# Kernel tuning notes

Measured on AMD Instinct MI355X. Metric: run time of the kernel, lower is better.

## Reference

```python
import jax, jax.numpy as jnp
import numpy as np

N = 50000      # nodes
E = 800000     # edges (before self loops)
F_IN = 512     # input feature dim (num_features)
D = 128        # hidden_dim
NBLK = 3       # num_layers - 1
EPS = 1e-5


def _layernorm(x, g, b):
    mu = x.mean(-1, keepdims=True)
    var = ((x - mu) ** 2).mean(-1, keepdims=True)
    return (x - mu) / jnp.sqrt(var + EPS) * g + b


def _gatv2(x, Wl, bl, Wr, br, att, bias, src, dst, n):
    # PyG GATv2Conv, heads=1, eval mode (attention dropout off), self loops in src/dst
    xl = x @ Wl + bl                      # [N, D] messages (x_j side)
    xr = x @ Wr + br                      # [N, D] target side (x_i)
    e = jax.nn.leaky_relu(xl[src] + xr[dst], negative_slope=0.2)  # [E', D]
    score = e @ att                       # [E']
    smax = jax.ops.segment_max(score, dst, num_segments=n)
    ex = jnp.exp(score - smax[dst])
    denom = jax.ops.segment_sum(ex, dst, num_segments=n)
    alpha = ex / denom[dst]               # segment softmax over incoming edges
    out = jax.ops.segment_sum(alpha[:, None] * xl[src], dst, num_segments=n)
    return out + bias


def setup_inputs() -> dict:
    key = jax.random.key(0)
    ks = jax.random.split(key, 32)
    w = lambda k, shape: (jax.random.normal(k, shape, jnp.float32) * 0.02)
    p = {}
    p["x"] = jax.random.normal(ks[0], (N, F_IN), jnp.float32)
    p["edge_index"] = jax.random.randint(ks[1], (2, E), 0, N)
    p["emb_W"] = w(ks[2], (F_IN, D)); p["emb_b"] = jnp.zeros((D,), jnp.float32)
    p["ln1_g"] = jnp.ones((NBLK, D), jnp.float32); p["ln1_b"] = jnp.zeros((NBLK, D), jnp.float32)
    p["gat_Wl"] = w(ks[3], (NBLK, D, D)); p["gat_bl"] = jnp.zeros((NBLK, D), jnp.float32)
    p["gat_Wr"] = w(ks[4], (NBLK, D, D)); p["gat_br"] = jnp.zeros((NBLK, D), jnp.float32)
    p["gat_att"] = w(ks[5], (NBLK, D)); p["gat_bias"] = jnp.zeros((NBLK, D), jnp.float32)
    for i in range(NBLK):
        h = D * (i + 1)  # mlp_ratio = level = i+1
        p[f"mlp_w1_{i}"] = w(ks[6 + 2 * i], (D, h))
        p[f"mlp_w2_{i}"] = w(ks[7 + 2 * i], (h, D))
    p["attn_Wa"] = w(ks[12], (D, D)); p["attn_ba"] = jnp.zeros((D,), jnp.float32)
    p["attn_Wb"] = w(ks[13], (D, D)); p["attn_bb"] = jnp.zeros((D,), jnp.float32)
    p["attn_Wc"] = w(ks[14], (D, 1)); p["attn_bc"] = jnp.zeros((1,), jnp.float32)
    p["rho_W"] = w(ks[15], (D, D)); p["rho_b"] = jnp.zeros((D,), jnp.float32)
    p["cls_W"] = w(ks[16], (D, 4)); p["cls_b"] = jnp.zeros((4,), jnp.float32)
    return p


def reference(x, edge_index, emb_W, emb_b, ln1_g, ln1_b, gat_Wl, gat_bl, gat_Wr, gat_br,
              gat_att, gat_bias, mlp_w1_0, mlp_w2_0, mlp_w1_1, mlp_w2_1, mlp_w1_2, mlp_w2_2,
              attn_Wa, attn_ba, attn_Wb, attn_bb, attn_Wc, attn_bc, rho_W, rho_b, cls_W, cls_b):
    n = x.shape[0]
    sl = jnp.arange(n, dtype=edge_index.dtype)
    src = jnp.concatenate([edge_index[0], sl])  # add self loops (GATv2Conv default)
    dst = jnp.concatenate([edge_index[1], sl])
    h = jax.nn.relu(x @ emb_W + emb_b)          # embedding (dropout off)
    mlps = [(mlp_w1_0, mlp_w2_0), (mlp_w1_1, mlp_w2_1), (mlp_w1_2, mlp_w2_2)]
    for i in range(NBLK):
        hn = _layernorm(h, ln1_g[i], ln1_b[i])
        h = h + _gatv2(hn, gat_Wl[i], gat_bl[i], gat_Wr[i], gat_br[i], gat_att[i], gat_bias[i], src, dst, n)
        w1, w2 = mlps[i]
        # NOTE: original forward applies channel_mix directly on x (norm2 is unused)
        h = h + jax.nn.gelu(h @ w1, approximate=False) @ w2
    # Attn_Net_Gated pooling
    a = jnp.tanh(h @ attn_Wa + attn_ba)
    b = jax.nn.sigmoid(h @ attn_Wb + attn_bb)
    A = ((a * b) @ attn_Wc + attn_bc).T          # [1, N]
    h_path = jax.nn.softmax(A, axis=1) @ h       # [1, D]
    hr = jax.nn.relu(h_path @ rho_W + rho_b)
    logits = hr @ cls_W + cls_b                  # [1, 4]
    Y_hat = jnp.argmax(logits, axis=1, keepdims=True)
    hazards = jax.nn.sigmoid(logits)
    S = jnp.cumprod(1.0 - hazards, axis=1)
    return (hazards, S, Y_hat, logits)
```

## Files before the change

kernel.cpp:

```cpp
#include <hip/hip_runtime.h>
#include <math.h>


#define D 128
#define NBLK 3
#define STG_STRIDE 132
#define S16 136
#define ROWS 128
#define BT 512

typedef __attribute__((ext_vector_type(8))) short bf16x8;
typedef __attribute__((ext_vector_type(4))) float f32x4;

static __device__ __forceinline__ float bf2f(unsigned short u) {
    union { unsigned i; float f; } c; c.i = ((unsigned)u) << 16; return c.f;
}
static __device__ __forceinline__ unsigned short f2bf(float f) {
    union { float f; unsigned i; } c; c.f = f;
    unsigned r = c.i + 0x7fff + ((c.i >> 16) & 1);
    return (unsigned short)(r >> 16);
}
static __device__ __forceinline__ void gl16(const unsigned short* g, unsigned short* l) {
    __builtin_amdgcn_global_load_lds((const __attribute__((address_space(1))) void*)g,
                                     (__attribute__((address_space(3))) void*)l, 16, 0, 0);
}
static __device__ __forceinline__ float gelu_f(float x) {
    return 0.5f * x * (1.f + erff(x * 0.70710678118654752f));
}

__global__ void zero_k(int* deg, int* fill, float* red, int n) {
    int i = blockIdx.x * blockDim.x + threadIdx.x;
    if (i < n) { deg[i] = 0; fill[i] = 0; }
    if (i < 132) red[i] = 0.f;
}

__global__ void hist_k(const int* __restrict__ dst, int* __restrict__ deg, int E) {
    int e = blockIdx.x * blockDim.x + threadIdx.x;
    if (e < E) atomicAdd(&deg[dst[e]], 1);
}

__global__ __launch_bounds__(256) void blockscan_k(const int* __restrict__ deg,
                                                   int* __restrict__ rowptr,
                                                   int* __restrict__ bsum, int n) {
    __shared__ int tmp[256];
    const int tid = threadIdx.x;
    const int i = blockIdx.x * 256 + tid;
    int v = (i < n) ? deg[i] : 0;
    tmp[tid] = v;
    __syncthreads();
#pragma unroll
    for (int off = 1; off < 256; off <<= 1) {
        int t = (tid >= off) ? tmp[tid - off] : 0;
        __syncthreads();
        tmp[tid] += t;
        __syncthreads();
    }
    if (i < n) rowptr[i + 1] = tmp[tid];
    if (tid == 255) bsum[blockIdx.x] = tmp[255];
}

__global__ __launch_bounds__(256) void scansums_k(int* __restrict__ bsum, int nb) {
    __shared__ int tmp[256];
    const int tid = threadIdx.x;
    int v = (tid < nb) ? bsum[tid] : 0;
    tmp[tid] = v;
    __syncthreads();
#pragma unroll
    for (int off = 1; off < 256; off <<= 1) {
        int t = (tid >= off) ? tmp[tid - off] : 0;
        __syncthreads();
        tmp[tid] += t;
        __syncthreads();
    }
    if (tid < nb) bsum[tid] = tmp[tid];
}

__global__ __launch_bounds__(256) void addoff_k(int* __restrict__ rowptr,
                                                const int* __restrict__ bsum, int n) {
    int i = blockIdx.x * 256 + threadIdx.x;
    if (i == 0) rowptr[0] = 0;
    if (i < n && blockIdx.x > 0) rowptr[i + 1] += bsum[blockIdx.x - 1];
}

__global__ void scatter_k(const int* __restrict__ src, const int* __restrict__ dst,
                          const int* __restrict__ rowptr, int* __restrict__ fill,
                          int* __restrict__ esrc, int E) {
    int e = blockIdx.x * blockDim.x + threadIdx.x;
    if (e < E) {
        int d = dst[e];
        int pos = rowptr[d] + atomicAdd(&fill[d], 1);
        esrc[pos] = src[e];
    }
}

struct WDesc { const float* s; unsigned short* d; int K; int M; };
struct WPack { WDesc w[21]; };

__global__ __launch_bounds__(256) void wprep_k(WPack p) {
    WDesc d = p.w[blockIdx.y];
    const int nc = d.K / 32;
    const int chunks = (d.M / 16) * nc * 64;
    for (int i = blockIdx.x * 256 + threadIdx.x; i < chunks; i += gridDim.x * 256) {
        const int l = i & 63;
        const int c = (i >> 6) % nc;
        const int t = i / (64 * nc);
        const int m = t * 16 + (l & 15);
        const int kb = c * 32 + ((l >> 4) & 3) * 8;
#pragma unroll
        for (int j = 0; j < 8; ++j)
            d.d[(size_t)i * 8 + j] = f2bf(d.s[(size_t)(kb + j) * d.M + m]);
    }
}

__global__ __launch_bounds__(256) void bcat_k(const float* bl, const float* br,
                                              const float* ba, const float* bb,
                                              float* sb) {
    const int t = threadIdx.x;
    for (int i = 0; i < 3; ++i)
        sb[i * 256 + t] = (t < 128) ? bl[i * 128 + t] : br[i * 128 + t - 128];
    sb[3 * 256 + t] = (t < 128) ? ba[t] : bb[t - 128];
}


static __device__ __forceinline__ void stage_blob(const unsigned short* src,
                                                  unsigned short* wls, int tid) {
#pragma unroll
    for (int i = 0; i < 4; ++i) {
        const int idx = i * BT + tid;
        gl16(src + (size_t)idx * 8, &wls[idx * 8]);
    }
}

static __device__ __forceinline__ void ln_row(float av[4][8], const float* lng,
                                              const float* lnb, int q) {
    float s = 0.f;
#pragma unroll
    for (int c = 0; c < 4; ++c)
#pragma unroll
        for (int j = 0; j < 8; ++j) s += av[c][j];
    s += __shfl_xor(s, 16, 64); s += __shfl_xor(s, 32, 64);
    const float mu = s * (1.f / 128.f);
    float vv = 0.f;
#pragma unroll
    for (int c = 0; c < 4; ++c)
#pragma unroll
        for (int j = 0; j < 8; ++j) { const float dd = av[c][j] - mu; vv += dd * dd; }
    vv += __shfl_xor(vv, 16, 64); vv += __shfl_xor(vv, 32, 64);
    const float rs = rsqrtf(vv * (1.f / 128.f) + 1e-5f);
#pragma unroll
    for (int c = 0; c < 4; ++c) {
        const int kb = c * 32 + q * 8;
        const float4 g0 = *(const float4*)(lng + kb);
        const float4 g1 = *(const float4*)(lng + kb + 4);
        const float4 b0 = *(const float4*)(lnb + kb);
        const float4 b1 = *(const float4*)(lnb + kb + 4);
        const float gg[8] = {g0.x, g0.y, g0.z, g0.w, g1.x, g1.y, g1.z, g1.w};
        const float bb[8] = {b0.x, b0.y, b0.z, b0.w, b1.x, b1.y, b1.z, b1.w};
#pragma unroll
        for (int j = 0; j < 8; ++j)
            av[c][j] = (av[c][j] - mu) * rs * gg[j] + bb[j];
    }
}

static __device__ __forceinline__ void gatproj(const bf16x8 xfr[4],
                                               const unsigned short* gatc,
                                               const float* sb256,
                                               unsigned short* X,
                                               unsigned short* wls,
                                               int rowbase, int w, int l, int N,
                                               int tid) {
    const int q = l >> 4, l15 = l & 15;
#pragma unroll
    for (int rnd = 0; rnd < 2; ++rnd) {
        __syncthreads();
        stage_blob(gatc + (size_t)rnd * 16384, wls, tid);
        f32x4 acc[8];
#pragma unroll
        for (int t = 0; t < 8; ++t) acc[t] = (f32x4){0.f, 0.f, 0.f, 0.f};
        __syncthreads();
#pragma unroll
        for (int c = 0; c < 4; ++c)
#pragma unroll
            for (int t = 0; t < 8; ++t) {
                const bf16x8 bfr = *(const bf16x8*)&wls[((t * 4 + c) * 64 + l) * 8];
                acc[t] = __builtin_amdgcn_mfma_f32_16x16x32_bf16(xfr[c], bfr, acc[t], 0, 0, 0);
            }
#pragma unroll
        for (int t = 0; t < 8; ++t) {
            const int col = rnd * 128 + t * 16 + l15;
            const float bv = sb256[col];
#pragma unroll
            for (int rr = 0; rr < 4; ++rr) {
                const int row = rowbase + w * 16 + q * 4 + rr;
                if (row < N) X[(size_t)row * 256 + col] = f2bf(acc[t][rr] + bv);
            }
        }
    }
}

__global__ __launch_bounds__(BT) void start_k(const float* __restrict__ x,
                                              const unsigned short* __restrict__ embc,
                                              const float* __restrict__ emb_b,
                                              const unsigned short* __restrict__ gatc,
                                              const float* __restrict__ lng,
                                              const float* __restrict__ lnb,
                                              const float* __restrict__ sb256,
                                              float* __restrict__ H,
                                              unsigned short* __restrict__ X, int N) {
    __shared__ __align__(16) char smem[ROWS * STG_STRIDE * 4];
    unsigned short* wls = (unsigned short*)smem;
    float* stg = (float*)smem;
    const int tid = threadIdx.x;
    const int w = tid >> 6, l = tid & 63, q = l >> 4, l15 = l & 15;
    const int rowbase = blockIdx.x * ROWS;
    int r = rowbase + w * 16 + l15;
    const bool rv = r < N; if (!rv) r = N - 1;

    f32x4 accH[8];
#pragma unroll
    for (int t = 0; t < 8; ++t) accH[t] = (f32x4){0.f, 0.f, 0.f, 0.f};

#pragma unroll
    for (int rnd = 0; rnd < 4; ++rnd) {
        if (rnd) __syncthreads();
        stage_blob(embc + (size_t)rnd * 16384, wls, tid);
        bf16x8 afr[4];
#pragma unroll
        for (int c = 0; c < 4; ++c) {
            const float* ap = x + (size_t)r * 512 + rnd * 128 + c * 32 + q * 8;
            const float4 v0 = *(const float4*)ap;
            const float4 v1 = *(const float4*)(ap + 4);
            afr[c][0] = (short)f2bf(v0.x); afr[c][1] = (short)f2bf(v0.y);
            afr[c][2] = (short)f2bf(v0.z); afr[c][3] = (short)f2bf(v0.w);
            afr[c][4] = (short)f2bf(v1.x); afr[c][5] = (short)f2bf(v1.y);
            afr[c][6] = (short)f2bf(v1.z); afr[c][7] = (short)f2bf(v1.w);
        }
        __syncthreads();
#pragma unroll
        for (int c = 0; c < 4; ++c)
#pragma unroll
            for (int t = 0; t < 8; ++t) {
                const bf16x8 bfr = *(const bf16x8*)&wls[((t * 4 + c) * 64 + l) * 8];
                accH[t] = __builtin_amdgcn_mfma_f32_16x16x32_bf16(afr[c], bfr, accH[t], 0, 0, 0);
            }
    }

    __syncthreads();
#pragma unroll
    for (int t = 0; t < 8; ++t) {
        const int col = t * 16 + l15;
        const float bv = emb_b[col];
#pragma unroll
        for (int rr = 0; rr < 4; ++rr) {
            const int row = rowbase + w * 16 + q * 4 + rr;
            const float hv = fmaxf(accH[t][rr] + bv, 0.f);
            if (row < N) H[(size_t)row * D + col] = hv;
            stg[(w * 16 + q * 4 + rr) * STG_STRIDE + col] = hv;
        }
    }
    __syncthreads();

    float av[4][8];
#pragma unroll
    for (int c = 0; c < 4; ++c)
#pragma unroll
        for (int j = 0; j < 8; ++j)
            av[c][j] = stg[(w * 16 + l15) * STG_STRIDE + c * 32 + q * 8 + j];
    ln_row(av, lng, lnb, q);
    bf16x8 xfr[4];
#pragma unroll
    for (int c = 0; c < 4; ++c)
#pragma unroll
        for (int j = 0; j < 8; ++j) xfr[c][j] = (short)f2bf(av[c][j]);

    gatproj(xfr, gatc, sb256, X, wls, rowbase, w, l, N, tid);
}

template <int NMR>
__global__ __launch_bounds__(BT) void bridge_k(float* __restrict__ H,
                                               const unsigned short* __restrict__ w1c,
                                               const unsigned short* __restrict__ w2c,
                                               const unsigned short* __restrict__ gatc,
                                               const float* __restrict__ lng,
                                               const float* __restrict__ lnb,
                                               const float* __restrict__ sb256,
                                               unsigned short* __restrict__ X, int N) {
    __shared__ __align__(16) char smem[ROWS * STG_STRIDE * 4];
    unsigned short* wls   = (unsigned short*)smem;
    unsigned short* stg16 = (unsigned short*)(smem + 32768);
    float*          stgF  = (float*)smem;
    const int tid = threadIdx.x;
    const int w = tid >> 6, l = tid & 63, q = l >> 4, l15 = l & 15;
    const int rowbase = blockIdx.x * ROWS;
    int r = rowbase + w * 16 + l15;
    const bool rv = r < N; if (!rv) r = N - 1;

    float av[4][8];
    bf16x8 afr[4];
#pragma unroll
    for (int c = 0; c < 4; ++c) {
        const float* ap = H + (size_t)r * D + c * 32 + q * 8;
        const float4 v0 = *(const float4*)ap;
        const float4 v1 = *(const float4*)(ap + 4);
        av[c][0] = v0.x; av[c][1] = v0.y; av[c][2] = v0.z; av[c][3] = v0.w;
        av[c][4] = v1.x; av[c][5] = v1.y; av[c][6] = v1.z; av[c][7] = v1.w;
#pragma unroll
        for (int j = 0; j < 8; ++j) afr[c][j] = (short)f2bf(av[c][j]);
    }

    f32x4 accH[8];
#pragma unroll
    for (int t = 0; t < 8; ++t) accH[t] = (f32x4){0.f, 0.f, 0.f, 0.f};

#pragma unroll
    for (int rnd = 0; rnd < NMR; ++rnd) {
        __syncthreads();
        stage_blob(w1c + (size_t)rnd * 16384, wls, tid);
        f32x4 accT[8];
#pragma unroll
        for (int t = 0; t < 8; ++t) accT[t] = (f32x4){0.f, 0.f, 0.f, 0.f};
        __syncthreads();
#pragma unroll
        for (int c = 0; c < 4; ++c)
#pragma unroll
            for (int t = 0; t < 8; ++t) {
                const bf16x8 bfr = *(const bf16x8*)&wls[((t * 4 + c) * 64 + l) * 8];
                accT[t] = __builtin_amdgcn_mfma_f32_16x16x32_bf16(afr[c], bfr, accT[t], 0, 0, 0);
            }
        __syncthreads();
#pragma unroll
        for (int t = 0; t < 8; ++t)
#pragma unroll
            for (int rr = 0; rr < 4; ++rr)
                stg16[(w * 16 + q * 4 + rr) * S16 + t * 16 + l15] = f2bf(gelu_f(accT[t][rr]));
        stage_blob(w2c + (size_t)rnd * 16384, wls, tid);
        __syncthreads();
        bf16x8 tfr[4];
#pragma unroll
        for (int c = 0; c < 4; ++c)
            tfr[c] = *(const bf16x8*)&stg16[(w * 16 + l15) * S16 + c * 32 + q * 8];
#pragma unroll
        for (int c = 0; c < 4; ++c)
#pragma unroll
            for (int t = 0; t < 8; ++t) {
                const bf16x8 bfr = *(const bf16x8*)&wls[((t * 4 + c) * 64 + l) * 8];
                accH[t] = __builtin_amdgcn_mfma_f32_16x16x32_bf16(tfr[c], bfr, accH[t], 0, 0, 0);
            }
    }

    __syncthreads();
#pragma unroll
    for (int t = 0; t < 8; ++t)
#pragma unroll
        for (int rr = 0; rr < 4; ++rr)
            stgF[(w * 16 + q * 4 + rr) * STG_STRIDE + t * 16 + l15] = accH[t][rr];
    __syncthreads();
#pragma unroll
    for (int c = 0; c < 4; ++c)
#pragma unroll
        for (int j = 0; j < 8; ++j)
            av[c][j] += stgF[(w * 16 + l15) * STG_STRIDE + c * 32 + q * 8 + j];

    if (rv) {
#pragma unroll
        for (int c = 0; c < 4; ++c) {
            float* hp = H + (size_t)r * D + c * 32 + q * 8;
            *(float4*)hp       = make_float4(av[c][0], av[c][1], av[c][2], av[c][3]);
            *(float4*)(hp + 4) = make_float4(av[c][4], av[c][5], av[c][6], av[c][7]);
        }
    }

    ln_row(av, lng, lnb, q);
    bf16x8 xfr[4];
#pragma unroll
    for (int c = 0; c < 4; ++c)
#pragma unroll
        for (int j = 0; j < 8; ++j) xfr[c][j] = (short)f2bf(av[c][j]);

    gatproj(xfr, gatc, sb256, X, wls, rowbase, w, l, N, tid);
}

__global__ __launch_bounds__(BT) void head_k(const float* __restrict__ H,
                                             const unsigned short* __restrict__ w1c,
                                             const unsigned short* __restrict__ w2c,
                                             const unsigned short* __restrict__ attc,
                                             const float* __restrict__ sb256,
                                             const float* __restrict__ Wc,
                                             const float* __restrict__ bc,
                                             float* __restrict__ red, int N) {
    __shared__ __align__(16) char smem[ROWS * STG_STRIDE * 4];
    unsigned short* wls   = (unsigned short*)smem;
    unsigned short* stg16 = (unsigned short*)(smem + 32768);
    float*          stgF  = (float*)smem;
    __shared__ float sacc[8][128];
    __shared__ float sdn[8];
    const int tid = threadIdx.x;
    const int w = tid >> 6, l = tid & 63, q = l >> 4, l15 = l & 15;
    const int rowbase = blockIdx.x * ROWS;
    int r = rowbase + w * 16 + l15;
    if (r > N - 1) r = N - 1;

    float av[4][8];
    bf16x8 afr[4];
#pragma unroll
    for (int c = 0; c < 4; ++c) {
        const float* ap = H + (size_t)r * D + c * 32 + q * 8;
        const float4 v0 = *(const float4*)ap;
        const float4 v1 = *(const float4*)(ap + 4);
        av[c][0] = v0.x; av[c][1] = v0.y; av[c][2] = v0.z; av[c][3] = v0.w;
        av[c][4] = v1.x; av[c][5] = v1.y; av[c][6] = v1.z; av[c][7] = v1.w;
#pragma unroll
        for (int j = 0; j < 8; ++j) afr[c][j] = (short)f2bf(av[c][j]);
    }

    f32x4 accH[8];
#pragma unroll
    for (int t = 0; t < 8; ++t) accH[t] = (f32x4){0.f, 0.f, 0.f, 0.f};

#pragma unroll
    for (int rnd = 0; rnd < 3; ++rnd) {
        __syncthreads();
        stage_blob(w1c + (size_t)rnd * 16384, wls, tid);
        f32x4 accT[8];
#pragma unroll
        for (int t = 0; t < 8; ++t) accT[t] = (f32x4){0.f, 0.f, 0.f, 0.f};
        __syncthreads();
#pragma unroll
        for (int c = 0; c < 4; ++c)
#pragma unroll
            for (int t = 0; t < 8; ++t) {
                const bf16x8 bfr = *(const bf16x8*)&wls[((t * 4 + c) * 64 + l) * 8];
                accT[t] = __builtin_amdgcn_mfma_f32_16x16x32_bf16(afr[c], bfr, accT[t], 0, 0, 0);
            }
        __syncthreads();
#pragma unroll
        for (int t = 0; t < 8; ++t)
#pragma unroll
            for (int rr = 0; rr < 4; ++rr)
                stg16[(w * 16 + q * 4 + rr) * S16 + t * 16 + l15] = f2bf(gelu_f(accT[t][rr]));
        stage_blob(w2c + (size_t)rnd * 16384, wls, tid);
        __syncthreads();
        bf16x8 tfr[4];
#pragma unroll
        for (int c = 0; c < 4; ++c)
            tfr[c] = *(const bf16x8*)&stg16[(w * 16 + l15) * S16 + c * 32 + q * 8];
#pragma unroll
        for (int c = 0; c < 4; ++c)
#pragma unroll
            for (int t = 0; t < 8; ++t) {
                const bf16x8 bfr = *(const bf16x8*)&wls[((t * 4 + c) * 64 + l) * 8];
                accH[t] = __builtin_amdgcn_mfma_f32_16x16x32_bf16(tfr[c], bfr, accH[t], 0, 0, 0);
            }
    }

    __syncthreads();
#pragma unroll
    for (int t = 0; t < 8; ++t)
#pragma unroll
        for (int rr = 0; rr < 4; ++rr)
            stgF[(w * 16 + q * 4 + rr) * STG_STRIDE + t * 16 + l15] = accH[t][rr];
    __syncthreads();
#pragma unroll
    for (int c = 0; c < 4; ++c)
#pragma unroll
        for (int j = 0; j < 8; ++j)
            av[c][j] += stgF[(w * 16 + l15) * STG_STRIDE + c * 32 + q * 8 + j];
#pragma unroll
    for (int c = 0; c < 4; ++c)
#pragma unroll
        for (int j = 0; j < 8; ++j) afr[c][j] = (short)f2bf(av[c][j]);

    float th[8][4];
    f32x4 acc[8];
#pragma unroll
    for (int rnd = 0; rnd < 2; ++rnd) {
        __syncthreads();
        stage_blob(attc + (size_t)rnd * 16384, wls, tid);
#pragma unroll
        for (int t = 0; t < 8; ++t) acc[t] = (f32x4){0.f, 0.f, 0.f, 0.f};
        __syncthreads();
#pragma unroll
        for (int c = 0; c < 4; ++c)
#pragma unroll
            for (int t = 0; t < 8; ++t) {
                const bf16x8 bfr = *(const bf16x8*)&wls[((t * 4 + c) * 64 + l) * 8];
                acc[t] = __builtin_amdgcn_mfma_f32_16x16x32_bf16(afr[c], bfr, acc[t], 0, 0, 0);
            }
        if (rnd == 0) {
#pragma unroll
            for (int t = 0; t < 8; ++t) {
                const float bv = sb256[t * 16 + l15];
#pragma unroll
                for (int rr = 0; rr < 4; ++rr) th[t][rr] = tanhf(acc[t][rr] + bv);
            }
        }
    }

    float pa[4] = {0.f, 0.f, 0.f, 0.f};
#pragma unroll
    for (int t = 0; t < 8; ++t) {
        const float bv = sb256[128 + t * 16 + l15];
        const float wcv = Wc[t * 16 + l15];
#pragma unroll
        for (int rr = 0; rr < 4; ++rr) {
            const float sg = 1.f / (1.f + __expf(-(acc[t][rr] + bv)));
            pa[rr] = fmaf(th[t][rr] * sg, wcv, pa[rr]);
        }
    }
#pragma unroll
    for (int m = 1; m < 16; m <<= 1)
#pragma unroll
        for (int rr = 0; rr < 4; ++rr) pa[rr] += __shfl_xor(pa[rr], m, 64);

    const float bcv = bc[0];
    float wgt[4];
#pragma unroll
    for (int rr = 0; rr < 4; ++rr) {
        const int row = rowbase + w * 16 + q * 4 + rr;
        wgt[rr] = (row < N) ? __expf(pa[rr] + bcv) : 0.f;
    }
    float s = wgt[0] + wgt[1] + wgt[2] + wgt[3];
    s += __shfl_xor(s, 16, 64);
    s += __shfl_xor(s, 32, 64);
    if (l == 0) sdn[w] = s;

    const int sl = ((l15 >> 2) << 4);
    float wv[4];
#pragma unroll
    for (int rr = 0; rr < 4; ++rr) wv[rr] = __shfl(wgt[rr], sl, 64);
    const int rsel = l15 & 3;
    const float wm = (rsel == 0) ? wv[0] : (rsel == 1) ? wv[1] : (rsel == 2) ? wv[2] : wv[3];

#pragma unroll
    for (int c = 0; c < 4; ++c) {
        float pv[8];
#pragma unroll
        for (int j = 0; j < 8; ++j) pv[j] = wm * av[c][j];
#pragma unroll
        for (int m = 1; m < 16; m <<= 1)
#pragma unroll
            for (int j = 0; j < 8; ++j) pv[j] += __shfl_xor(pv[j], m, 64);
        if (l15 == 0) {
#pragma unroll
            for (int j = 0; j < 8; ++j) sacc[w][c * 32 + q * 8 + j] = pv[j];
        }
    }
    __syncthreads();
    if (tid < 128) {
        float tot = 0.f;
#pragma unroll
        for (int ww = 0; ww < 8; ++ww) tot += sacc[ww][tid];
        atomicAdd(&red[tid], tot);
    }
    if (tid == 0) {
        float ds = 0.f;
#pragma unroll
        for (int ww = 0; ww < 8; ++ww) ds += sdn[ww];
        atomicAdd(&red[128], ds);
    }
}

__global__ __launch_bounds__(256) void gat3_k(const unsigned short* __restrict__ X,
                                              const float* __restrict__ att,
                                              const float* __restrict__ gbias,
                                              const int* __restrict__ rowptr,
                                              const int* __restrict__ esrc,
                                              float* __restrict__ H, int n) {
    const int l = threadIdx.x & 63;
    const int node = blockIdx.x * 4 + (threadIdx.x >> 6);
    if (node >= n) return;
    const int q = l >> 4;
    const int d0 = (l & 15) * 8;

    float a8[8], xr[8], xs[8];
    {
        const float4 t0 = *(const float4*)&att[d0];
        const float4 t1 = *(const float4*)&att[d0 + 4];
        a8[0] = t0.x; a8[1] = t0.y; a8[2] = t0.z; a8[3] = t0.w;
        a8[4] = t1.x; a8[5] = t1.y; a8[6] = t1.z; a8[7] = t1.w;
        const bf16x8 uxs = *(const bf16x8*)&X[(size_t)node * 256 + d0];
        const bf16x8 uxr = *(const bf16x8*)&X[(size_t)node * 256 + 128 + d0];
#pragma unroll
        for (int j = 0; j < 8; ++j) {
            xs[j] = bf2f((unsigned short)uxs[j]);
            xr[j] = bf2f((unsigned short)uxr[j]);
        }
    }

    float sc = 0.f;
#pragma unroll
    for (int j = 0; j < 8; ++j) {
        const float e = xs[j] + xr[j];
        sc = fmaf(a8[j], fmaxf(e, 0.2f * e), sc);
    }
#pragma unroll
    for (int m = 1; m < 16; m <<= 1) sc += __shfl_xor(sc, m, 64);
    const float wself = __expf(sc);
    float dsum = (q == 0) ? wself : 0.f;
    float acc[8];
#pragma unroll
    for (int j = 0; j < 8; ++j) acc[j] = (q == 0) ? wself * xs[j] : 0.f;

    const int p1 = rowptr[node + 1];
    int p = rowptr[node] + q;
    bool v0 = p < p1, v1 = p + 4 < p1, v2 = p + 8 < p1;
    int i2 = v2 ? esrc[p + 8] : 0;
    bf16x8 u0, u1;
    if (v0) u0 = *(const bf16x8*)&X[(size_t)esrc[p] * 256 + d0];
    if (v1) u1 = *(const bf16x8*)&X[(size_t)esrc[p + 4] * 256 + d0];
    while (v0) {
        bf16x8 u2;
        if (v2) u2 = *(const bf16x8*)&X[(size_t)i2 * 256 + d0];
        const bool v3 = p + 12 < p1;
        const int i3 = v3 ? esrc[p + 12] : 0;

        float xl[8];
#pragma unroll
        for (int j = 0; j < 8; ++j) xl[j] = bf2f((unsigned short)u0[j]);
        float e_sc = 0.f;
#pragma unroll
        for (int j = 0; j < 8; ++j) {
            const float e = xl[j] + xr[j];
            e_sc = fmaf(a8[j], fmaxf(e, 0.2f * e), e_sc);
        }
#pragma unroll
        for (int m = 1; m < 16; m <<= 1) e_sc += __shfl_xor(e_sc, m, 64);
        const float wgt = __expf(e_sc);
        dsum += wgt;
#pragma unroll
        for (int j = 0; j < 8; ++j) acc[j] = fmaf(wgt, xl[j], acc[j]);

        u0 = u1; u1 = u2; i2 = i3;
        v0 = v1; v1 = v2; v2 = v3;
        p += 4;
    }

#pragma unroll
    for (int m = 16; m < 64; m <<= 1) {
        dsum += __shfl_xor(dsum, m, 64);
#pragma unroll
        for (int j = 0; j < 8; ++j) acc[j] += __shfl_xor(acc[j], m, 64);
    }

    if (q == 0) {
        const float inv = 1.f / dsum;
        const size_t o = (size_t)node * D + d0;
        float4 h0 = *(const float4*)&H[o];
        float4 h1 = *(const float4*)&H[o + 4];
        float hv[8] = {h0.x, h0.y, h0.z, h0.w, h1.x, h1.y, h1.z, h1.w};
#pragma unroll
        for (int j = 0; j < 8; ++j) hv[j] += acc[j] * inv + gbias[d0 + j];
        *(float4*)&H[o]     = make_float4(hv[0], hv[1], hv[2], hv[3]);
        *(float4*)&H[o + 4] = make_float4(hv[4], hv[5], hv[6], hv[7]);
    }
}

__global__ __launch_bounds__(128) void final_k(const float* __restrict__ red,
                                               const float* __restrict__ rho_W,
                                               const float* __restrict__ rho_b,
                                               const float* __restrict__ cls_W,
                                               const float* __restrict__ cls_b,
                                               float* __restrict__ out) {
    __shared__ float hp[128];
    __shared__ float hr[128];
    __shared__ float lg[4];
    const int t = threadIdx.x;
    hp[t] = red[t] / red[128];
    __syncthreads();
    float s = rho_b[t];
    for (int k = 0; k < 128; ++k) s = fmaf(hp[k], rho_W[k * 128 + t], s);
    hr[t] = fmaxf(s, 0.f);
    __syncthreads();
    if (t < 4) {
        float l = cls_b[t];
        for (int k = 0; k < 128; ++k) l = fmaf(hr[k], cls_W[k * 4 + t], l);
        lg[t] = l;
    }
    __syncthreads();
    if (t == 0) {
        float hz[4], S[4];
        for (int c = 0; c < 4; ++c) hz[c] = 1.f / (1.f + expf(-lg[c]));
        S[0] = 1.f - hz[0];
        for (int c = 1; c < 4; ++c) S[c] = S[c - 1] * (1.f - hz[c]);
        int am = 0; float bm = lg[0];
        for (int c = 1; c < 4; ++c) if (lg[c] > bm) { bm = lg[c]; am = c; }
        out[0] = hz[0]; out[1] = hz[1]; out[2] = hz[2]; out[3] = hz[3];
        out[4] = S[0];  out[5] = S[1];  out[6] = S[2];  out[7] = S[3];
        out[8] = (float)am;
        out[9] = lg[0]; out[10] = lg[1]; out[11] = lg[2]; out[12] = lg[3];
    }
}

static inline int cdiv(int a, int b) { return (a + b - 1) / b; }

extern "C" void kernel_launch(void* const* d_in, const int* in_sizes, int n_in,
                              void* d_out, int out_size, void* d_ws, size_t ws_size,
                              hipStream_t stream) {
    const float* x      = (const float*)d_in[0];
    const int*   ei     = (const int*)d_in[1];
    const float* emb_W  = (const float*)d_in[2];
    const float* emb_b  = (const float*)d_in[3];
    const float* ln1_g  = (const float*)d_in[4];
    const float* ln1_b  = (const float*)d_in[5];
    const float* gat_Wl = (const float*)d_in[6];
    const float* gat_bl = (const float*)d_in[7];
    const float* gat_Wr = (const float*)d_in[8];
    const float* gat_br = (const float*)d_in[9];
    const float* gat_att  = (const float*)d_in[10];
    const float* gat_bias = (const float*)d_in[11];
    const float* mlp_w1[NBLK] = {(const float*)d_in[12], (const float*)d_in[14], (const float*)d_in[16]};
    const float* mlp_w2[NBLK] = {(const float*)d_in[13], (const float*)d_in[15], (const float*)d_in[17]};
    const float* attn_Wa = (const float*)d_in[18];
    const float* attn_ba = (const float*)d_in[19];
    const float* attn_Wb = (const float*)d_in[20];
    const float* attn_bb = (const float*)d_in[21];
    const float* attn_Wc = (const float*)d_in[22];
    const float* attn_bc = (const float*)d_in[23];
    const float* rho_W   = (const float*)d_in[24];
    const float* rho_b   = (const float*)d_in[25];
    const float* cls_W   = (const float*)d_in[26];
    const float* cls_b   = (const float*)d_in[27];
    float* out = (float*)d_out;

    const int N = in_sizes[0] / 512;
    const int E = in_sizes[1] / 2;
    const int* src = ei;
    const int* dst = ei + E;
    const int gx = cdiv(N, ROWS);

    char* base = (char*)d_ws;
    float* H = (float*)base;
    unsigned short* X = (unsigned short*)(H + (size_t)N * D);
    float* red  = (float*)(X + (size_t)N * 256);
    float* sb   = red + 132;
    unsigned short* wbuf = (unsigned short*)(sb + 1024);
    int* esrc   = (int*)(wbuf + 393216);
    int* deg    = esrc + E;
    int* rowptr = deg + N;
    int* fill   = rowptr + N + 1;
    int* bsum   = fill + N;

    unsigned short* embT = wbuf;
    unsigned short* gatT = wbuf + 4 * 16384;
    unsigned short* w1T0 = gatT + 6 * 16384;
    unsigned short* w1T1 = w1T0 + 16384;
    unsigned short* w1T2 = w1T1 + 2 * 16384;
    unsigned short* w2T0 = w1T2 + 3 * 16384;
    unsigned short* w2T1 = w2T0 + 16384;
    unsigned short* w2T2 = w2T1 + 2 * 16384;
    unsigned short* attT = w2T2 + 3 * 16384;
    unsigned short* w1T[NBLK] = {w1T0, w1T1, w1T2};
    unsigned short* w2T[NBLK] = {w2T0, w2T1, w2T2};

    const int nb = cdiv(N, 256);
    zero_k<<<cdiv(N, 256), 256, 0, stream>>>(deg, fill, red, N);
    hist_k<<<cdiv(E, 256), 256, 0, stream>>>(dst, deg, E);
    blockscan_k<<<nb, 256, 0, stream>>>(deg, rowptr, bsum, N);
    scansums_k<<<1, 256, 0, stream>>>(bsum, nb);
    addoff_k<<<nb, 256, 0, stream>>>(rowptr, bsum, N);
    scatter_k<<<cdiv(E, 256), 256, 0, stream>>>(src, dst, rowptr, fill, esrc, E);

    {
        WPack p;
        int di = 0;
        for (int r = 0; r < 4; ++r)
            p.w[di++] = {emb_W + (size_t)r * 128 * 128, embT + (size_t)r * 16384, 128, 128};
        for (int i = 0; i < 3; ++i) {
            p.w[di++] = {gat_Wl + (size_t)i * 16384, gatT + (size_t)(2 * i) * 16384, 128, 128};
            p.w[di++] = {gat_Wr + (size_t)i * 16384, gatT + (size_t)(2 * i + 1) * 16384, 128, 128};
        }
        for (int i = 0; i < 3; ++i)
            p.w[di++] = {mlp_w1[i], w1T[i], 128, 128 * (i + 1)};
        for (int i = 0; i < 3; ++i)
            for (int r = 0; r <= i; ++r)
                p.w[di++] = {mlp_w2[i] + (size_t)r * 128 * 128, w2T[i] + (size_t)r * 16384, 128, 128};
        p.w[di++] = {attn_Wa, attT, 128, 128};
        p.w[di++] = {attn_Wb, attT + 16384, 128, 128};
        wprep_k<<<dim3(32, 21), 256, 0, stream>>>(p);
    }
    bcat_k<<<1, 256, 0, stream>>>(gat_bl, gat_br, attn_ba, attn_bb, sb);

    start_k<<<gx, BT, 0, stream>>>(x, embT, emb_b, gatT, ln1_g, ln1_b, sb, H, X, N);
    gat3_k<<<cdiv(N, 4), 256, 0, stream>>>(X, gat_att, gat_bias, rowptr, esrc, H, N);

    bridge_k<1><<<gx, BT, 0, stream>>>(H, w1T[0], w2T[0], gatT + 2 * 16384,
                                       ln1_g + D, ln1_b + D, sb + 256, X, N);
    gat3_k<<<cdiv(N, 4), 256, 0, stream>>>(X, gat_att + D, gat_bias + D, rowptr, esrc, H, N);

    bridge_k<2><<<gx, BT, 0, stream>>>(H, w1T[1], w2T[1], gatT + 4 * 16384,
                                       ln1_g + 2 * D, ln1_b + 2 * D, sb + 512, X, N);
    gat3_k<<<cdiv(N, 4), 256, 0, stream>>>(X, gat_att + 2 * D, gat_bias + 2 * D, rowptr, esrc, H, N);

    head_k<<<gx, BT, 0, stream>>>(H, w1T[2], w2T[2], attT, sb + 3 * 256,
                                  attn_Wc, attn_bc, red, N);
    final_k<<<1, 128, 0, stream>>>(red, rho_W, rho_b, cls_W, cls_b, out);
}
```

Measured before the change: 646.0 us.

## Prefetch next weight blob into registers while current MFMA stage runs

Replaces the synchronous global-to-LDS weight staging in the embedding, MLP and head kernels with register prefetch. The next 32KB weight chunk is loaded into registers while the current chunk is consumed by MFMAs, then committed to LDS between barriers. This hides the latency of global weight loads behind compute. The cost is 16 extra VGPRs per thread for the prefetch buffer, which may hurt occupancy at 512 threads, and some extra barriers.

```diff
diff --git a/kernel.cpp b/kernel.cpp
--- a/kernel.cpp
+++ b/kernel.cpp
@@ -131,6 +131,31 @@
     }
 }
 
+static __device__ __forceinline__ void pf_issue(const unsigned short* src, int tid,
+                                                float4 pf[4]) {
+#pragma unroll
+    for (int i = 0; i < 4; ++i)
+        pf[i] = *(const float4*)(src + (size_t)(i * BT + tid) * 8);
+}
+static __device__ __forceinline__ void pf_commit(unsigned short* wls, int tid,
+                                                 const float4 pf[4]) {
+#pragma unroll
+    for (int i = 0; i < 4; ++i)
+        *(float4*)(&wls[(i * BT + tid) * 8]) = pf[i];
+}
+
+static __device__ __forceinline__ void mfma32(const bf16x8 a[4],
+                                              const unsigned short* wls,
+                                              int l, f32x4 acc[8]) {
+#pragma unroll
+    for (int c = 0; c < 4; ++c)
+#pragma unroll
+        for (int t = 0; t < 8; ++t) {
+            const bf16x8 bfr = *(const bf16x8*)&wls[((t * 4 + c) * 64 + l) * 8];
+            acc[t] = __builtin_amdgcn_mfma_f32_16x16x32_bf16(a[c], bfr, acc[t], 0, 0, 0);
+        }
+}
+
 static __device__ __forceinline__ void ln_row(float av[4][8], const float* lng,
                                               const float* lnb, int q) {
     float s = 0.f;
@@ -162,38 +187,17 @@
     }
 }
 
-static __device__ __forceinline__ void gatproj(const bf16x8 xfr[4],
-                                               const unsigned short* gatc,
-                                               const float* sb256,
-                                               unsigned short* X,
-                                               unsigned short* wls,
-                                               int rowbase, int w, int l, int N,
-                                               int tid) {
-    const int q = l >> 4, l15 = l & 15;
-#pragma unroll
-    for (int rnd = 0; rnd < 2; ++rnd) {
-        __syncthreads();
-        stage_blob(gatc + (size_t)rnd * 16384, wls, tid);
-        f32x4 acc[8];
-#pragma unroll
-        for (int t = 0; t < 8; ++t) acc[t] = (f32x4){0.f, 0.f, 0.f, 0.f};
-        __syncthreads();
-#pragma unroll
-        for (int c = 0; c < 4; ++c)
-#pragma unroll
-            for (int t = 0; t < 8; ++t) {
-                const bf16x8 bfr = *(const bf16x8*)&wls[((t * 4 + c) * 64 + l) * 8];
-                acc[t] = __builtin_amdgcn_mfma_f32_16x16x32_bf16(xfr[c], bfr, acc[t], 0, 0, 0);
-            }
-#pragma unroll
-        for (int t = 0; t < 8; ++t) {
-            const int col = rnd * 128 + t * 16 + l15;
-            const float bv = sb256[col];
-#pragma unroll
-            for (int rr = 0; rr < 4; ++rr) {
-                const int row = rowbase + w * 16 + q * 4 + rr;
-                if (row < N) X[(size_t)row * 256 + col] = f2bf(acc[t][rr] + bv);
-            }
+static __device__ __forceinline__ void xwrite(const f32x4 acc[8], const float* sb256,
+                                              unsigned short* X, int rnd, int rowbase,
+                                              int w, int q, int l15, int N) {
+#pragma unroll
+    for (int t = 0; t < 8; ++t) {
+        const int col = rnd * 128 + t * 16 + l15;
+        const float bv = sb256[col];
+#pragma unroll
+        for (int rr = 0; rr < 4; ++rr) {
+            const int row = rowbase + w * 16 + q * 4 + rr;
+            if (row < N) X[(size_t)row * 256 + col] = f2bf(acc[t][rr] + bv);
         }
     }
 }
@@ -215,15 +219,19 @@
     const int rowbase = blockIdx.x * ROWS;
     int r = rowbase + w * 16 + l15;
     const bool rv = r < N; if (!rv) r = N - 1;
+    float4 pf[4];
 
     f32x4 accH[8];
 #pragma unroll
     for (int t = 0; t < 8; ++t) accH[t] = (f32x4){0.f, 0.f, 0.f, 0.f};
 
+    stage_blob(embc, wls, tid);
+    __syncthreads();
+
 #pragma unroll
     for (int rnd = 0; rnd < 4; ++rnd) {
-        if (rnd) __syncthreads();
-        stage_blob(embc + (size_t)rnd * 16384, wls, tid);
+        const unsigned short* nb = (rnd < 3) ? embc + (size_t)(rnd + 1) * 16384 : gatc;
+        pf_issue(nb, tid, pf);
         bf16x8 afr[4];
 #pragma unroll
         for (int c = 0; c < 4; ++c) {
@@ -235,17 +243,11 @@
             afr[c][4] = (short)f2bf(v1.x); afr[c][5] = (short)f2bf(v1.y);
             afr[c][6] = (short)f2bf(v1.z); afr[c][7] = (short)f2bf(v1.w);
         }
-        __syncthreads();
-#pragma unroll
-        for (int c = 0; c < 4; ++c)
-#pragma unroll
-            for (int t = 0; t < 8; ++t) {
-                const bf16x8 bfr = *(const bf16x8*)&wls[((t * 4 + c) * 64 + l) * 8];
-                accH[t] = __builtin_amdgcn_mfma_f32_16x16x32_bf16(afr[c], bfr, accH[t], 0, 0, 0);
-            }
-    }
-
-    __syncthreads();
+        mfma32(afr, wls, l, accH);
+        __syncthreads();
+        if (rnd < 3) { pf_commit(wls, tid, pf); __syncthreads(); }
+    }
+
 #pragma unroll
     for (int t = 0; t < 8; ++t) {
         const int col = t * 16 + l15;
@@ -258,8 +260,6 @@
             stg[(w * 16 + q * 4 + rr) * STG_STRIDE + col] = hv;
         }
     }
-    __syncthreads();
-
     float av[4][8];
 #pragma unroll
     for (int c = 0; c < 4; ++c)
@@ -273,7 +273,24 @@
 #pragma unroll
         for (int j = 0; j < 8; ++j) xfr[c][j] = (short)f2bf(av[c][j]);
 
-    gatproj(xfr, gatc, sb256, X, wls, rowbase, w, l, N, tid);
+    __syncthreads();
+    pf_commit(wls, tid, pf);
+    __syncthreads();
+
+    pf_issue(gatc + 16384, tid, pf);
+    f32x4 acc[8];
+#pragma unroll
+    for (int t = 0; t < 8; ++t) acc[t] = (f32x4){0.f, 0.f, 0.f, 0.f};
+    mfma32(xfr, wls, l, acc);
+    xwrite(acc, sb256, X, 0, rowbase, w, q, l15, N);
+    __syncthreads();
+    pf_commit(wls, tid, pf);
+    __syncthreads();
+
+#pragma unroll
+    for (int t = 0; t < 8; ++t) acc[t] = (f32x4){0.f, 0.f, 0.f, 0.f};
+    mfma32(xfr, wls, l, acc);
+    xwrite(acc, sb256, X, 1, rowbase, w, q, l15, N);
 }
 
 template <int NMR>
@@ -294,6 +311,9 @@
     const int rowbase = blockIdx.x * ROWS;
     int r = rowbase + w * 16 + l15;
     const bool rv = r < N; if (!rv) r = N - 1;
+    float4 pf[4];
+
+    stage_blob(w1c, wls, tid);
 
     float av[4][8];
     bf16x8 afr[4];
@@ -311,50 +331,39 @@
     f32x4 accH[8];
 #pragma unroll
     for (int t = 0; t < 8; ++t) accH[t] = (f32x4){0.f, 0.f, 0.f, 0.f};
+    __syncthreads();
 
 #pragma unroll
     for (int rnd = 0; rnd < NMR; ++rnd) {
-        __syncthreads();
-        stage_blob(w1c + (size_t)rnd * 16384, wls, tid);
+        pf_issue(w2c + (size_t)rnd * 16384, tid, pf);
         f32x4 accT[8];
 #pragma unroll
         for (int t = 0; t < 8; ++t) accT[t] = (f32x4){0.f, 0.f, 0.f, 0.f};
-        __syncthreads();
-#pragma unroll
-        for (int c = 0; c < 4; ++c)
-#pragma unroll
-            for (int t = 0; t < 8; ++t) {
-                const bf16x8 bfr = *(const bf16x8*)&wls[((t * 4 + c) * 64 + l) * 8];
-                accT[t] = __builtin_amdgcn_mfma_f32_16x16x32_bf16(afr[c], bfr, accT[t], 0, 0, 0);
-            }
-        __syncthreads();
+        mfma32(afr, wls, l, accT);
 #pragma unroll
         for (int t = 0; t < 8; ++t)
 #pragma unroll
             for (int rr = 0; rr < 4; ++rr)
                 stg16[(w * 16 + q * 4 + rr) * S16 + t * 16 + l15] = f2bf(gelu_f(accT[t][rr]));
-        stage_blob(w2c + (size_t)rnd * 16384, wls, tid);
-        __syncthreads();
+        __syncthreads();
+        pf_commit(wls, tid, pf);
+        __syncthreads();
+        const unsigned short* nb = (rnd + 1 < NMR) ? w1c + (size_t)(rnd + 1) * 16384 : gatc;
+        pf_issue(nb, tid, pf);
         bf16x8 tfr[4];
 #pragma unroll
         for (int c = 0; c < 4; ++c)
             tfr[c] = *(const bf16x8*)&stg16[(w * 16 + l15) * S16 + c * 32 + q * 8];
-#pragma unroll
-        for (int c = 0; c < 4; ++c)
-#pragma unroll
-            for (int t = 0; t < 8; ++t) {
-                const bf16x8 bfr = *(const bf16x8*)&wls[((t * 4 + c) * 64 + l) * 8];
-                accH[t] = __builtin_amdgcn_mfma_f32_16x16x32_bf16(tfr[c], bfr, accH[t], 0, 0, 0);
-            }
-    }
-
-    __syncthreads();
+        mfma32(tfr, wls, l, accH);
+        __syncthreads();
+        if (rnd + 1 < NMR) { pf_commit(wls, tid, pf); __syncthreads(); }
+    }
+
 #pragma unroll
     for (int t = 0; t < 8; ++t)
 #pragma unroll
         for (int rr = 0; rr < 4; ++rr)
             stgF[(w * 16 + q * 4 + rr) * STG_STRIDE + t * 16 + l15] = accH[t][rr];
-    __syncthreads();
 #pragma unroll
     for (int c = 0; c < 4; ++c)
 #pragma unroll
@@ -377,7 +386,24 @@
 #pragma unroll
         for (int j = 0; j < 8; ++j) xfr[c][j] = (short)f2bf(av[c][j]);
 
-    gatproj(xfr, gatc, sb256, X, wls, rowbase, w, l, N, tid);
+    __syncthreads();
+    pf_commit(wls, tid, pf);
+    __syncthreads();
+
+    pf_issue(gatc + 16384, tid, pf);
+    f32x4 acc[8];
+#pragma unroll
+    for (int t = 0; t < 8; ++t) acc[t] = (f32x4){0.f, 0.f, 0.f, 0.f};
+    mfma32(xfr, wls, l, acc);
+    xwrite(acc, sb256, X, 0, rowbase, w, q, l15, N);
+    __syncthreads();
+    pf_commit(wls, tid, pf);
+    __syncthreads();
+
+#pragma unroll
+    for (int t = 0; t < 8; ++t) acc[t] = (f32x4){0.f, 0.f, 0.f, 0.f};
+    mfma32(xfr, wls, l, acc);
+    xwrite(acc, sb256, X, 1, rowbase, w, q, l15, N);
 }
 
 __global__ __launch_bounds__(BT) void head_k(const float* __restrict__ H,
@@ -399,6 +425,9 @@
     const int rowbase = blockIdx.x * ROWS;
     int r = rowbase + w * 16 + l15;
     if (r > N - 1) r = N - 1;
+    float4 pf[4];
+
+    stage_blob(w1c, wls, tid);
 
     float av[4][8];
     bf16x8 afr[4];
@@ -416,50 +445,39 @@
     f32x4 accH[8];
 #pragma unroll
     for (int t = 0; t < 8; ++t) accH[t] = (f32x4){0.f, 0.f, 0.f, 0.f};
+    __syncthreads();
 
 #pragma unroll
     for (int rnd = 0; rnd < 3; ++rnd) {
-        __syncthreads();
-        stage_blob(w1c + (size_t)rnd * 16384, wls, tid);
+        pf_issue(w2c + (size_t)rnd * 16384, tid, pf);
         f32x4 accT[8];
 #pragma unroll
         for (int t = 0; t < 8; ++t) accT[t] = (f32x4){0.f, 0.f, 0.f, 0.f};
-        __syncthreads();
-#pragma unroll
-        for (int c = 0; c < 4; ++c)
-#pragma unroll
-            for (int t = 0; t < 8; ++t) {
-                const bf16x8 bfr = *(const bf16x8*)&wls[((t * 4 + c) * 64 + l) * 8];
-                accT[t] = __builtin_amdgcn_mfma_f32_16x16x32_bf16(afr[c], bfr, accT[t], 0, 0, 0);
-            }
-        __syncthreads();
+        mfma32(afr, wls, l, accT);
 #pragma unroll
         for (int t = 0; t < 8; ++t)
 #pragma unroll
             for (int rr = 0; rr < 4; ++rr)
                 stg16[(w * 16 + q * 4 + rr) * S16 + t * 16 + l15] = f2bf(gelu_f(accT[t][rr]));
-        stage_blob(w2c + (size_t)rnd * 16384, wls, tid);
-        __syncthreads();
+        __syncthreads();
+        pf_commit(wls, tid, pf);
+        __syncthreads();
+        const unsigned short* nb = (rnd + 1 < 3) ? w1c + (size_t)(rnd + 1) * 16384 : attc;
+        pf_issue(nb, tid, pf);
         bf16x8 tfr[4];
 #pragma unroll
         for (int c = 0; c < 4; ++c)
             tfr[c] = *(const bf16x8*)&stg16[(w * 16 + l15) * S16 + c * 32 + q * 8];
-#pragma unroll
-        for (int c = 0; c < 4; ++c)
-#pragma unroll
-            for (int t = 0; t < 8; ++t) {
-                const bf16x8 bfr = *(const bf16x8*)&wls[((t * 4 + c) * 64 + l) * 8];
-                accH[t] = __builtin_amdgcn_mfma_f32_16x16x32_bf16(tfr[c], bfr, accH[t], 0, 0, 0);
-            }
-    }
-
-    __syncthreads();
+        mfma32(tfr, wls, l, accH);
+        __syncthreads();
+        if (rnd + 1 < 3) { pf_commit(wls, tid, pf); __syncthreads(); }
+    }
+
 #pragma unroll
     for (int t = 0; t < 8; ++t)
 #pragma unroll
         for (int rr = 0; rr < 4; ++rr)
             stgF[(w * 16 + q * 4 + rr) * STG_STRIDE + t * 16 + l15] = accH[t][rr];
-    __syncthreads();
 #pragma unroll
     for (int c = 0; c < 4; ++c)
 #pragma unroll
@@ -470,31 +488,29 @@
 #pragma unroll
         for (int j = 0; j < 8; ++j) afr[c][j] = (short)f2bf(av[c][j]);
 
+    __syncthreads();
+    pf_commit(wls, tid, pf);
+    __syncthreads();
+
+    pf_issue(attc + 16384, tid, pf);
     float th[8][4];
     f32x4 acc[8];
 #pragma unroll
-    for (int rnd = 0; rnd < 2; ++rnd) {
-        __syncthreads();
-        stage_blob(attc + (size_t)rnd * 16384, wls, tid);
-#pragma unroll
-        for (int t = 0; t < 8; ++t) acc[t] = (f32x4){0.f, 0.f, 0.f, 0.f};
-        __syncthreads();
-#pragma unroll
-        for (int c = 0; c < 4; ++c)
-#pragma unroll
-            for (int t = 0; t < 8; ++t) {
-                const bf16x8 bfr = *(const bf16x8*)&wls[((t * 4 + c) * 64 + l) * 8];
-                acc[t] = __builtin_amdgcn_mfma_f32_16x16x32_bf16(afr[c], bfr, acc[t], 0, 0, 0);
-            }
-        if (rnd == 0) {
-#pragma unroll
-            for (int t = 0; t < 8; ++t) {
-                const float bv = sb256[t * 16 + l15];
-#pragma unroll
-                for (int rr = 0; rr < 4; ++rr) th[t][rr] = tanhf(acc[t][rr] + bv);
-            }
-        }
-    }
+    for (int t = 0; t < 8; ++t) acc[t] = (f32x4){0.f, 0.f, 0.f, 0.f};
+    mfma32(afr, wls, l, acc);
+#pragma unroll
+    for (int t = 0; t < 8; ++t) {
+        const float bv = sb256[t * 16 + l15];
+#pragma unroll
+        for (int rr = 0; rr < 4; ++rr) th[t][rr] = tanhf(acc[t][rr] + bv);
+    }
+    __syncthreads();
+    pf_commit(wls, tid, pf);
+    __syncthreads();
+
+#pragma unroll
+    for (int t = 0; t < 8; ++t) acc[t] = (f32x4){0.f, 0.f, 0.f, 0.f};
+    mfma32(afr, wls, l, acc);
 
     float pa[4] = {0.f, 0.f, 0.f, 0.f};
 #pragma unroll
```

Result: slower. 713.5 us (+10.4%).
